# Kernel tuning notes

Measured on AMD Instinct MI355X. Metric: run time of the kernel, lower is better.

The kernel has to match this reference:

```python
import math
import jax, jax.numpy as jnp
import numpy as np

HEAD_DIM = 64
CAUSAL = True


def setup_inputs() -> dict:
    key = jax.random.key(0)
    kq, kk, kv = jax.random.split(key, 3)
    q = jax.random.normal(kq, (2, 16, 1024, HEAD_DIM), dtype=jnp.float32)
    k = jax.random.normal(kk, (2, 16, 8192, HEAD_DIM), dtype=jnp.float32)
    v = jax.random.normal(kv, (2, 16, 8192, HEAD_DIM), dtype=jnp.float32)
    return {"q": q, "k": k, "v": v, "q_chunk_start": 7168}


def reference(q, k, v, q_chunk_start):
    # q: (B, nh, Tq, dh); k, v: (B, nh, Tk, dh)
    Tq = q.shape[2]
    Tk = k.shape[2]
    scale = math.sqrt(HEAD_DIM)
    # scores: (B, nh, Tq, Tk)
    scores = jnp.einsum("bhqd,bhkd->bhqk", q, k) / scale
    if CAUSAL:
        q_pos = jnp.arange(Tq) + q_chunk_start          # (Tq,)
        k_pos = jnp.arange(Tk)                          # (Tk,)
        mask = k_pos[None, :] > q_pos[:, None]          # (Tq, Tk) True = masked
        scores = jnp.where(mask, -jnp.inf, scores)
    attn = jax.nn.softmax(scores, axis=-1)
    attn = jnp.nan_to_num(attn, nan=0.0)                # fully-masked rows -> 0
    return jnp.einsum("bhqk,bhkd->bhqd", attn, v)
```

## Files before the change

kernel.cpp:

```cpp
#include <hip/hip_runtime.h>
#include <hip/hip_bf16.h>

#define TQ 1024
#define TK 8192
#define DH 64
#define NBH 32
#define QT 64
#define KT 64
#define NW 4

typedef __attribute__((ext_vector_type(8))) short short8;
typedef __attribute__((ext_vector_type(4))) short short4v;
typedef __attribute__((ext_vector_type(4))) float f32x4;

static __device__ __forceinline__ short f2bf(float f) {
  __hip_bfloat16 h = __float2bfloat16(f);
  return __builtin_bit_cast(short, h);
}

__global__ __launch_bounds__(256, 2)
void attn_fwd(const float* __restrict__ qg,
              const float* __restrict__ kg,
              const float* __restrict__ vg,
              const int* __restrict__ qcs_p,
              float* __restrict__ outg)
{
  __shared__ __align__(16) short Klds[KT * DH];
  __shared__ __align__(16) short Vt[DH * KT];
  __shared__ __align__(16) short Plds[NW][16 * KT];

  const int tid  = threadIdx.x;
  const int wave = tid >> 6;
  const int lane = tid & 63;
  const int lg   = lane >> 4;
  const int li   = lane & 15;

  const int bid = blockIdx.x;
  const int bh  = bid & (NBH - 1);
  const int qt  = bid >> 5;
  const int qcs = *qcs_p;

  const int q_base = qt * QT;
  const int wrow   = wave * 16;

  const float* qp = qg + ((size_t)bh * TQ + q_base + wrow) * DH;
  const float* kp = kg + (size_t)bh * TK * DH;
  const float* vp = vg + (size_t)bh * TK * DH;

  const float qscale = 0.125f * 1.44269504088896f;
  short8 qf[2];
  #pragma unroll
  for (int h = 0; h < 2; ++h) {
    const float* src = qp + li * DH + h * 32 + lg * 8;
    float4 a = *(const float4*)(src);
    float4 b = *(const float4*)(src + 4);
    short8 f;
    f[0] = f2bf(a.x * qscale); f[1] = f2bf(a.y * qscale);
    f[2] = f2bf(a.z * qscale); f[3] = f2bf(a.w * qscale);
    f[4] = f2bf(b.x * qscale); f[5] = f2bf(b.y * qscale);
    f[6] = f2bf(b.z * qscale); f[7] = f2bf(b.w * qscale);
    qf[h] = f;
  }

  f32x4 o[4];
  #pragma unroll
  for (int ct = 0; ct < 4; ++ct) o[ct] = (f32x4){0.f, 0.f, 0.f, 0.f};
  float rm[4], rl[4];
  #pragma unroll
  for (int r = 0; r < 4; ++r) { rm[r] = -1e30f; rl[r] = 0.f; }

  const int lim    = qcs + q_base + QT;
  const int n_keys = lim < TK ? lim : TK;
  const int n_tiles = (n_keys + KT - 1) / KT;

  const int t_key = tid >> 4;
  const int t_d   = (tid & 15) * 4;

  for (int tile = 0; tile < n_tiles; ++tile) {
    const int kt0 = tile * KT;

    #pragma unroll
    for (int it = 0; it < 4; ++it) {
      const int key = t_key + it * 16;
      const size_t goff = (size_t)(kt0 + key) * DH + t_d;
      float4 kv = *(const float4*)(kp + goff);
      short4v ks;
      ks[0] = f2bf(kv.x); ks[1] = f2bf(kv.y);
      ks[2] = f2bf(kv.z); ks[3] = f2bf(kv.w);
      int e = (key * DH + t_d) ^ ((key & 7) << 3);
      *(short4v*)(&Klds[e]) = ks;

      float4 vv = *(const float4*)(vp + goff);
      short vs0 = f2bf(vv.x), vs1 = f2bf(vv.y), vs2 = f2bf(vv.z), vs3 = f2bf(vv.w);
      int d0 = t_d;
      Vt[((d0 + 0) * KT + key) ^ (((d0 + 0) & 7) << 3)] = vs0;
      Vt[((d0 + 1) * KT + key) ^ (((d0 + 1) & 7) << 3)] = vs1;
      Vt[((d0 + 2) * KT + key) ^ (((d0 + 2) & 7) << 3)] = vs2;
      Vt[((d0 + 3) * KT + key) ^ (((d0 + 3) & 7) << 3)] = vs3;
    }
    __syncthreads();

    f32x4 s[4];
    #pragma unroll
    for (int t = 0; t < 4; ++t) {
      f32x4 acc = (f32x4){0.f, 0.f, 0.f, 0.f};
      #pragma unroll
      for (int h = 0; h < 2; ++h) {
        int e = ((t * 16 + li) * DH + h * 32 + lg * 8) ^ ((li & 7) << 3);
        short8 kf = *(const short8*)(&Klds[e]);
        acc = __builtin_amdgcn_mfma_f32_16x16x32_bf16(qf[h], kf, acc, 0, 0, 0);
      }
      s[t] = acc;
    }

    if (kt0 + KT - 1 > qcs + q_base + wrow) {
      #pragma unroll
      for (int t = 0; t < 4; ++t) {
        const int keyg = kt0 + t * 16 + li;
        #pragma unroll
        for (int r = 0; r < 4; ++r) {
          const int qpos = qcs + q_base + wrow + lg * 4 + r;
          if (keyg > qpos) s[t][r] = -INFINITY;
        }
      }
    }

    float al[4], mn[4];
    #pragma unroll
    for (int r = 0; r < 4; ++r) {
      float tm = fmaxf(fmaxf(s[0][r], s[1][r]), fmaxf(s[2][r], s[3][r]));
      #pragma unroll
      for (int off = 1; off < 16; off <<= 1)
        tm = fmaxf(tm, __shfl_xor(tm, off, 64));
      float m2 = fmaxf(rm[r], tm);
      al[r] = __builtin_amdgcn_exp2f(rm[r] - m2);
      mn[r] = m2;
      rm[r] = m2;
    }

    float ps[4] = {0.f, 0.f, 0.f, 0.f};
    #pragma unroll
    for (int t = 0; t < 4; ++t) {
      #pragma unroll
      for (int r = 0; r < 4; ++r) {
        float p = __builtin_amdgcn_exp2f(s[t][r] - mn[r]);
        ps[r] += p;
        const int row = lg * 4 + r;
        Plds[wave][(row * KT + t * 16 + li) ^ ((row & 7) << 3)] = f2bf(p);
      }
    }

    #pragma unroll
    for (int r = 0; r < 4; ++r) {
      float sum = ps[r];
      #pragma unroll
      for (int off = 1; off < 16; off <<= 1)
        sum += __shfl_xor(sum, off, 64);
      rl[r] = rl[r] * al[r] + sum;
      #pragma unroll
      for (int ct = 0; ct < 4; ++ct) o[ct][r] *= al[r];
    }

    #pragma unroll
    for (int sk = 0; sk < 2; ++sk) {
      int ep = (li * KT + sk * 32 + lg * 8) ^ ((li & 7) << 3);
      short8 pf = *(const short8*)(&Plds[wave][ep]);
      #pragma unroll
      for (int ct = 0; ct < 4; ++ct) {
        int ev = ((ct * 16 + li) * KT + sk * 32 + lg * 8) ^ ((li & 7) << 3);
        short8 vf = *(const short8*)(&Vt[ev]);
        o[ct] = __builtin_amdgcn_mfma_f32_16x16x32_bf16(pf, vf, o[ct], 0, 0, 0);
      }
    }
    __syncthreads();
  }

  float* op = outg + ((size_t)bh * TQ + q_base + wrow) * DH;
  #pragma unroll
  for (int r = 0; r < 4; ++r) {
    const float inv = rl[r] > 0.f ? 1.0f / rl[r] : 0.f;
    #pragma unroll
    for (int ct = 0; ct < 4; ++ct) {
      op[(lg * 4 + r) * DH + ct * 16 + li] = o[ct][r] * inv;
    }
  }
}

extern "C" void kernel_launch(void* const* d_in, const int* in_sizes, int n_in,
                              void* d_out, int out_size, void* d_ws, size_t ws_size,
                              hipStream_t stream) {
  const float* q   = (const float*)d_in[0];
  const float* k   = (const float*)d_in[1];
  const float* v   = (const float*)d_in[2];
  const int*   qcs = (const int*)d_in[3];
  float* out = (float*)d_out;

  dim3 grid(NBH * (TQ / QT));
  dim3 block(256);
  attn_fwd<<<grid, block, 0, stream>>>(q, k, v, qcs, out);
}
```

Before: 438.4 us.

## Split key dimension into four chunks with a separate combine kernel

Turns the attention into a split-K (flash-decoding style) scheme. Each block handles one quarter of the key range and writes unnormalized partial outputs plus row max and sum to workspace, and a second kernel merges them with log-sum-exp weights. The aim is to raise the grid from 512 to 2048 blocks so the GPU stays busy, since each block otherwise walks up to 8192 keys serially. It also raises the occupancy hint in launch bounds and changes the V-transpose LDS swizzle to cut bank conflicts. The cost is extra workspace traffic and a second launch, with a fallback to the old single-kernel path when the workspace is too small.

Measured after the change: 945.7 us. 2.16x slower.

```diff
diff --git a/kernel.cpp b/kernel.cpp
--- a/kernel.cpp
+++ b/kernel.cpp
@@ -8,6 +8,7 @@
 #define QT 64
 #define KT 64
 #define NW 4
+#define ROWS (NBH * TQ)
 
 typedef __attribute__((ext_vector_type(8))) short short8;
 typedef __attribute__((ext_vector_type(4))) short short4v;
@@ -18,12 +19,15 @@
   return __builtin_bit_cast(short, h);
 }
 
-__global__ __launch_bounds__(256, 2)
+template<int NS, bool PART>
+__global__ __launch_bounds__(256, 6)
 void attn_fwd(const float* __restrict__ qg,
               const float* __restrict__ kg,
               const float* __restrict__ vg,
               const int* __restrict__ qcs_p,
-              float* __restrict__ outg)
+              float* __restrict__ outg,
+              float* __restrict__ mpart,
+              float* __restrict__ lpart)
 {
   __shared__ __align__(16) short Klds[KT * DH];
   __shared__ __align__(16) short Vt[DH * KT];
@@ -37,11 +41,14 @@
 
   const int bid = blockIdx.x;
   const int bh  = bid & (NBH - 1);
-  const int qt  = bid >> 5;
+  const int s   = (bid >> 5) & (NS - 1);
+  const int qt  = bid >> (5 + (NS == 4 ? 2 : 0));
   const int qcs = *qcs_p;
 
   const int q_base = qt * QT;
   const int wrow   = wave * 16;
+  const int chunk_start = s * (TK / NS);
+  const int chunk_end   = chunk_start + (TK / NS);
 
   const float* qp = qg + ((size_t)bh * TQ + q_base + wrow) * DH;
   const float* kp = kg + (size_t)bh * TK * DH;
@@ -69,15 +76,15 @@
   #pragma unroll
   for (int r = 0; r < 4; ++r) { rm[r] = -1e30f; rl[r] = 0.f; }
 
-  const int lim    = qcs + q_base + QT;
-  const int n_keys = lim < TK ? lim : TK;
-  const int n_tiles = (n_keys + KT - 1) / KT;
+  int lim = qcs + q_base + QT;
+  if (lim > chunk_end) lim = chunk_end;
+  const int n_tiles = (lim - chunk_start + KT - 1) / KT;
 
   const int t_key = tid >> 4;
   const int t_d   = (tid & 15) * 4;
 
   for (int tile = 0; tile < n_tiles; ++tile) {
-    const int kt0 = tile * KT;
+    const int kt0 = chunk_start + tile * KT;
 
     #pragma unroll
     for (int it = 0; it < 4; ++it) {
@@ -93,14 +100,14 @@
       float4 vv = *(const float4*)(vp + goff);
       short vs0 = f2bf(vv.x), vs1 = f2bf(vv.y), vs2 = f2bf(vv.z), vs3 = f2bf(vv.w);
       int d0 = t_d;
-      Vt[((d0 + 0) * KT + key) ^ (((d0 + 0) & 7) << 3)] = vs0;
-      Vt[((d0 + 1) * KT + key) ^ (((d0 + 1) & 7) << 3)] = vs1;
-      Vt[((d0 + 2) * KT + key) ^ (((d0 + 2) & 7) << 3)] = vs2;
-      Vt[((d0 + 3) * KT + key) ^ (((d0 + 3) & 7) << 3)] = vs3;
+      Vt[((d0 + 0) * KT + key) ^ ((((d0 + 0) >> 1) & 7) << 3)] = vs0;
+      Vt[((d0 + 1) * KT + key) ^ ((((d0 + 1) >> 1) & 7) << 3)] = vs1;
+      Vt[((d0 + 2) * KT + key) ^ ((((d0 + 2) >> 1) & 7) << 3)] = vs2;
+      Vt[((d0 + 3) * KT + key) ^ ((((d0 + 3) >> 1) & 7) << 3)] = vs3;
     }
     __syncthreads();
 
-    f32x4 s[4];
+    f32x4 sv[4];
     #pragma unroll
     for (int t = 0; t < 4; ++t) {
       f32x4 acc = (f32x4){0.f, 0.f, 0.f, 0.f};
@@ -110,7 +117,7 @@
         short8 kf = *(const short8*)(&Klds[e]);
         acc = __builtin_amdgcn_mfma_f32_16x16x32_bf16(qf[h], kf, acc, 0, 0, 0);
       }
-      s[t] = acc;
+      sv[t] = acc;
     }
 
     if (kt0 + KT - 1 > qcs + q_base + wrow) {
@@ -120,7 +127,7 @@
         #pragma unroll
         for (int r = 0; r < 4; ++r) {
           const int qpos = qcs + q_base + wrow + lg * 4 + r;
-          if (keyg > qpos) s[t][r] = -INFINITY;
+          if (keyg > qpos) sv[t][r] = -INFINITY;
         }
       }
     }
@@ -128,7 +135,7 @@
     float al[4], mn[4];
     #pragma unroll
     for (int r = 0; r < 4; ++r) {
-      float tm = fmaxf(fmaxf(s[0][r], s[1][r]), fmaxf(s[2][r], s[3][r]));
+      float tm = fmaxf(fmaxf(sv[0][r], sv[1][r]), fmaxf(sv[2][r], sv[3][r]));
       #pragma unroll
       for (int off = 1; off < 16; off <<= 1)
         tm = fmaxf(tm, __shfl_xor(tm, off, 64));
@@ -143,7 +150,7 @@
     for (int t = 0; t < 4; ++t) {
       #pragma unroll
       for (int r = 0; r < 4; ++r) {
-        float p = __builtin_amdgcn_exp2f(s[t][r] - mn[r]);
+        float p = __builtin_amdgcn_exp2f(sv[t][r] - mn[r]);
         ps[r] += p;
         const int row = lg * 4 + r;
         Plds[wave][(row * KT + t * 16 + li) ^ ((row & 7) << 3)] = f2bf(p);
@@ -167,7 +174,8 @@
       short8 pf = *(const short8*)(&Plds[wave][ep]);
       #pragma unroll
       for (int ct = 0; ct < 4; ++ct) {
-        int ev = ((ct * 16 + li) * KT + sk * 32 + lg * 8) ^ ((li & 7) << 3);
+        int d = ct * 16 + li;
+        int ev = (d * KT + sk * 32 + lg * 8) ^ (((d >> 1) & 7) << 3);
         short8 vf = *(const short8*)(&Vt[ev]);
         o[ct] = __builtin_amdgcn_mfma_f32_16x16x32_bf16(pf, vf, o[ct], 0, 0, 0);
       }
@@ -175,15 +183,58 @@
     __syncthreads();
   }
 
-  float* op = outg + ((size_t)bh * TQ + q_base + wrow) * DH;
-  #pragma unroll
-  for (int r = 0; r < 4; ++r) {
-    const float inv = rl[r] > 0.f ? 1.0f / rl[r] : 0.f;
-    #pragma unroll
-    for (int ct = 0; ct < 4; ++ct) {
-      op[(lg * 4 + r) * DH + ct * 16 + li] = o[ct][r] * inv;
-    }
-  }
+  if constexpr (PART) {
+    float* opr = outg + (((size_t)s * NBH + bh) * TQ + q_base + wrow) * DH;
+    const size_t rbase = ((size_t)s * NBH + bh) * TQ + q_base + wrow;
+    #pragma unroll
+    for (int r = 0; r < 4; ++r) {
+      #pragma unroll
+      for (int ct = 0; ct < 4; ++ct)
+        opr[(lg * 4 + r) * DH + ct * 16 + li] = o[ct][r];
+      if (li == 0) {
+        mpart[rbase + lg * 4 + r] = rm[r];
+        lpart[rbase + lg * 4 + r] = rl[r];
+      }
+    }
+  } else {
+    float* op = outg + ((size_t)bh * TQ + q_base + wrow) * DH;
+    #pragma unroll
+    for (int r = 0; r < 4; ++r) {
+      const float inv = rl[r] > 0.f ? 1.0f / rl[r] : 0.f;
+      #pragma unroll
+      for (int ct = 0; ct < 4; ++ct)
+        op[(lg * 4 + r) * DH + ct * 16 + li] = o[ct][r] * inv;
+    }
+  }
+}
+
+template<int NS>
+__global__ __launch_bounds__(256)
+void combine(const float* __restrict__ opart,
+             const float* __restrict__ mp,
+             const float* __restrict__ lp,
+             float* __restrict__ outg)
+{
+  const int gid = blockIdx.x * 256 + threadIdx.x;
+  const int rg = gid >> 6;
+  const int d  = gid & 63;
+
+  float m[NS], l[NS];
+  float M = -1e30f;
+  #pragma unroll
+  for (int s = 0; s < NS; ++s) {
+    m[s] = mp[(size_t)s * ROWS + rg];
+    l[s] = lp[(size_t)s * ROWS + rg];
+    M = fmaxf(M, m[s]);
+  }
+  float L = 0.f, acc = 0.f;
+  #pragma unroll
+  for (int s = 0; s < NS; ++s) {
+    float w = __builtin_amdgcn_exp2f(m[s] - M);
+    L += w * l[s];
+    acc += w * opart[((size_t)s * ROWS + rg) * DH + d];
+  }
+  outg[(size_t)rg * DH + d] = L > 0.f ? acc / L : 0.f;
 }
 
 extern "C" void kernel_launch(void* const* d_in, const int* in_sizes, int n_in,
@@ -195,7 +246,20 @@
   const int*   qcs = (const int*)d_in[3];
   float* out = (float*)d_out;
 
-  dim3 grid(NBH * (TQ / QT));
-  dim3 block(256);
-  attn_fwd<<<grid, block, 0, stream>>>(q, k, v, qcs, out);
-}
+  constexpr int    NS = 4;
+  constexpr size_t O_ELEMS  = (size_t)NS * ROWS * DH;
+  constexpr size_t ML_ELEMS = (size_t)NS * ROWS;
+  constexpr size_t WS_NEED  = (O_ELEMS + 2 * ML_ELEMS) * sizeof(float);
+
+  if (ws_size >= WS_NEED) {
+    float* opart = (float*)d_ws;
+    float* mpart = opart + O_ELEMS;
+    float* lpart = mpart + ML_ELEMS;
+    dim3 grid(NBH * NS * (TQ / QT));
+    attn_fwd<NS, true><<<grid, dim3(256), 0, stream>>>(q, k, v, qcs, opart, mpart, lpart);
+    combine<NS><<<dim3(ROWS * DH / 256), dim3(256), 0, stream>>>(opart, mpart, lpart, out);
+  } else {
+    dim3 grid(NBH * (TQ / QT));
+    attn_fwd<1, false><<<grid, dim3(256), 0, stream>>>(q, k, v, qcs, out, nullptr, nullptr);
+  }
+}
```

## Pre-convert K/V to swizzled bf16 tiles and double-buffer via global_load_lds

Applied to the files above, without the earlier changes.

Adds a prep kernel that converts K and V from fp32 to bf16 once, writing each 64x64 tile in the final swizzled LDS layout (V transposed) into workspace. The main kernel then streams the tiles straight into double-buffered LDS with global_load_lds, prefetching the next tile during compute, and raises wave priority around the MFMA sections. This removes the repeated per-block fp32 loads and conversions (each K/V tile is reread by 16 query-tile blocks) and overlaps memory with compute. The cost is an extra kernel launch plus writing and rereading a bf16 copy, and doubled K/V LDS use. A fallback path with a different V swizzle is kept for when workspace is too small.

New measurement: 383.0 us. 1.14x faster.

```diff
diff --git a/kernel.cpp b/kernel.cpp
--- a/kernel.cpp
+++ b/kernel.cpp
@@ -8,6 +8,8 @@
 #define QT 64
 #define KT 64
 #define NW 4
+#define NTILE (TK / KT)
+#define TILE_E (KT * DH)
 
 typedef __attribute__((ext_vector_type(8))) short short8;
 typedef __attribute__((ext_vector_type(4))) short short4v;
@@ -18,15 +20,58 @@
   return __builtin_bit_cast(short, h);
 }
 
+#define GLD16(gsrc, ldst)                                                     \
+  __builtin_amdgcn_global_load_lds(                                           \
+      (const __attribute__((address_space(1))) unsigned int*)(gsrc),          \
+      (__attribute__((address_space(3))) unsigned int*)(ldst), 16, 0, 0)
+
+__global__ __launch_bounds__(256)
+void prep(const float* __restrict__ kg, const float* __restrict__ vg,
+          short* __restrict__ Kg2, short* __restrict__ Vg2)
+{
+  __shared__ __align__(16) short Ki[TILE_E];
+  __shared__ __align__(16) short Vi[TILE_E];
+  const int bid = blockIdx.x;
+  const int h = bid >> 7, t = bid & (NTILE - 1);
+  const int tid = threadIdx.x;
+  const int t_key = tid >> 4;
+  const int t_d   = (tid & 15) * 4;
+
+  const float* kp = kg + ((size_t)h * TK + (size_t)t * KT) * DH;
+  const float* vp = vg + ((size_t)h * TK + (size_t)t * KT) * DH;
+
+  #pragma unroll
+  for (int it = 0; it < 4; ++it) {
+    const int key = t_key + it * 16;
+    float4 kv = *(const float4*)(kp + key * DH + t_d);
+    short4v ks;
+    ks[0] = f2bf(kv.x); ks[1] = f2bf(kv.y); ks[2] = f2bf(kv.z); ks[3] = f2bf(kv.w);
+    *(short4v*)(&Ki[(key * 64 + t_d) ^ ((key & 7) << 3)]) = ks;
+
+    float4 vv = *(const float4*)(vp + key * DH + t_d);
+    Vi[((t_d + 0) * 64 + key) ^ (((t_d + 0) & 7) << 3)] = f2bf(vv.x);
+    Vi[((t_d + 1) * 64 + key) ^ (((t_d + 1) & 7) << 3)] = f2bf(vv.y);
+    Vi[((t_d + 2) * 64 + key) ^ (((t_d + 2) & 7) << 3)] = f2bf(vv.z);
+    Vi[((t_d + 3) * 64 + key) ^ (((t_d + 3) & 7) << 3)] = f2bf(vv.w);
+  }
+  __syncthreads();
+
+  const size_t base = (size_t)bid * TILE_E;
+  *(short8*)(&Kg2[base + tid * 16])     = *(short8*)(&Ki[tid * 16]);
+  *(short8*)(&Kg2[base + tid * 16 + 8]) = *(short8*)(&Ki[tid * 16 + 8]);
+  *(short8*)(&Vg2[base + tid * 16])     = *(short8*)(&Vi[tid * 16]);
+  *(short8*)(&Vg2[base + tid * 16 + 8]) = *(short8*)(&Vi[tid * 16 + 8]);
+}
+
 __global__ __launch_bounds__(256, 2)
-void attn_fwd(const float* __restrict__ qg,
-              const float* __restrict__ kg,
-              const float* __restrict__ vg,
-              const int* __restrict__ qcs_p,
-              float* __restrict__ outg)
+void attn_main(const float* __restrict__ qg,
+               const short* __restrict__ Kg2,
+               const short* __restrict__ Vg2,
+               const int* __restrict__ qcs_p,
+               float* __restrict__ outg)
 {
-  __shared__ __align__(16) short Klds[KT * DH];
-  __shared__ __align__(16) short Vt[DH * KT];
+  __shared__ __align__(16) short Kb[2][TILE_E];
+  __shared__ __align__(16) short Vb[2][TILE_E];
   __shared__ __align__(16) short Plds[NW][16 * KT];
 
   const int tid  = threadIdx.x;
@@ -44,8 +89,7 @@
   const int wrow   = wave * 16;
 
   const float* qp = qg + ((size_t)bh * TQ + q_base + wrow) * DH;
-  const float* kp = kg + (size_t)bh * TK * DH;
-  const float* vp = vg + (size_t)bh * TK * DH;
+  const size_t tile_base0 = (size_t)bh * NTILE * TILE_E;
 
   const float qscale = 0.125f * 1.44269504088896f;
   short8 qf[2];
@@ -73,45 +117,38 @@
   const int n_keys = lim < TK ? lim : TK;
   const int n_tiles = (n_keys + KT - 1) / KT;
 
-  const int t_key = tid >> 4;
-  const int t_d   = (tid & 15) * 4;
+  const int chunk = wave * 2;
+
+  auto stage = [&](int b, int tile) {
+    const size_t tb = tile_base0 + (size_t)tile * TILE_E;
+    GLD16(Kg2 + tb + (chunk + 0) * 512 + lane * 8, &Kb[b][(chunk + 0) * 512]);
+    GLD16(Kg2 + tb + (chunk + 1) * 512 + lane * 8, &Kb[b][(chunk + 1) * 512]);
+    GLD16(Vg2 + tb + (chunk + 0) * 512 + lane * 8, &Vb[b][(chunk + 0) * 512]);
+    GLD16(Vg2 + tb + (chunk + 1) * 512 + lane * 8, &Vb[b][(chunk + 1) * 512]);
+  };
+
+  stage(0, 0);
+  __syncthreads();
+  int buf = 0;
 
   for (int tile = 0; tile < n_tiles; ++tile) {
     const int kt0 = tile * KT;
-
-    #pragma unroll
-    for (int it = 0; it < 4; ++it) {
-      const int key = t_key + it * 16;
-      const size_t goff = (size_t)(kt0 + key) * DH + t_d;
-      float4 kv = *(const float4*)(kp + goff);
-      short4v ks;
-      ks[0] = f2bf(kv.x); ks[1] = f2bf(kv.y);
-      ks[2] = f2bf(kv.z); ks[3] = f2bf(kv.w);
-      int e = (key * DH + t_d) ^ ((key & 7) << 3);
-      *(short4v*)(&Klds[e]) = ks;
-
-      float4 vv = *(const float4*)(vp + goff);
-      short vs0 = f2bf(vv.x), vs1 = f2bf(vv.y), vs2 = f2bf(vv.z), vs3 = f2bf(vv.w);
-      int d0 = t_d;
-      Vt[((d0 + 0) * KT + key) ^ (((d0 + 0) & 7) << 3)] = vs0;
-      Vt[((d0 + 1) * KT + key) ^ (((d0 + 1) & 7) << 3)] = vs1;
-      Vt[((d0 + 2) * KT + key) ^ (((d0 + 2) & 7) << 3)] = vs2;
-      Vt[((d0 + 3) * KT + key) ^ (((d0 + 3) & 7) << 3)] = vs3;
-    }
-    __syncthreads();
-
-    f32x4 s[4];
+    if (tile + 1 < n_tiles) stage(buf ^ 1, tile + 1);
+
+    f32x4 sv[4];
+    __builtin_amdgcn_s_setprio(1);
     #pragma unroll
     for (int t = 0; t < 4; ++t) {
       f32x4 acc = (f32x4){0.f, 0.f, 0.f, 0.f};
       #pragma unroll
       for (int h = 0; h < 2; ++h) {
-        int e = ((t * 16 + li) * DH + h * 32 + lg * 8) ^ ((li & 7) << 3);
-        short8 kf = *(const short8*)(&Klds[e]);
+        int e = ((t * 16 + li) * 64 + h * 32 + lg * 8) ^ ((li & 7) << 3);
+        short8 kf = *(const short8*)(&Kb[buf][e]);
         acc = __builtin_amdgcn_mfma_f32_16x16x32_bf16(qf[h], kf, acc, 0, 0, 0);
       }
-      s[t] = acc;
-    }
+      sv[t] = acc;
+    }
+    __builtin_amdgcn_s_setprio(0);
 
     if (kt0 + KT - 1 > qcs + q_base + wrow) {
       #pragma unroll
@@ -120,7 +157,7 @@
         #pragma unroll
         for (int r = 0; r < 4; ++r) {
           const int qpos = qcs + q_base + wrow + lg * 4 + r;
-          if (keyg > qpos) s[t][r] = -INFINITY;
+          if (keyg > qpos) sv[t][r] = -INFINITY;
         }
       }
     }
@@ -128,7 +165,7 @@
     float al[4], mn[4];
     #pragma unroll
     for (int r = 0; r < 4; ++r) {
-      float tm = fmaxf(fmaxf(s[0][r], s[1][r]), fmaxf(s[2][r], s[3][r]));
+      float tm = fmaxf(fmaxf(sv[0][r], sv[1][r]), fmaxf(sv[2][r], sv[3][r]));
       #pragma unroll
       for (int off = 1; off < 16; off <<= 1)
         tm = fmaxf(tm, __shfl_xor(tm, off, 64));
@@ -143,7 +180,7 @@
     for (int t = 0; t < 4; ++t) {
       #pragma unroll
       for (int r = 0; r < 4; ++r) {
-        float p = __builtin_amdgcn_exp2f(s[t][r] - mn[r]);
+        float p = __builtin_amdgcn_exp2f(sv[t][r] - mn[r]);
         ps[r] += p;
         const int row = lg * 4 + r;
         Plds[wave][(row * KT + t * 16 + li) ^ ((row & 7) << 3)] = f2bf(p);
@@ -165,9 +202,176 @@
     for (int sk = 0; sk < 2; ++sk) {
       int ep = (li * KT + sk * 32 + lg * 8) ^ ((li & 7) << 3);
       short8 pf = *(const short8*)(&Plds[wave][ep]);
+      __builtin_amdgcn_s_setprio(1);
       #pragma unroll
       for (int ct = 0; ct < 4; ++ct) {
-        int ev = ((ct * 16 + li) * KT + sk * 32 + lg * 8) ^ ((li & 7) << 3);
+        int e = ((ct * 16 + li) * 64 + sk * 32 + lg * 8) ^ ((li & 7) << 3);
+        short8 vf = *(const short8*)(&Vb[buf][e]);
+        o[ct] = __builtin_amdgcn_mfma_f32_16x16x32_bf16(pf, vf, o[ct], 0, 0, 0);
+      }
+      __builtin_amdgcn_s_setprio(0);
+    }
+
+    __syncthreads();
+    buf ^= 1;
+  }
+
+  float* op = outg + ((size_t)bh * TQ + q_base + wrow) * DH;
+  #pragma unroll
+  for (int r = 0; r < 4; ++r) {
+    const float inv = rl[r] > 0.f ? 1.0f / rl[r] : 0.f;
+    #pragma unroll
+    for (int ct = 0; ct < 4; ++ct)
+      op[(lg * 4 + r) * DH + ct * 16 + li] = o[ct][r] * inv;
+  }
+}
+
+__global__ __launch_bounds__(256, 2)
+void attn_fallback(const float* __restrict__ qg,
+                   const float* __restrict__ kg,
+                   const float* __restrict__ vg,
+                   const int* __restrict__ qcs_p,
+                   float* __restrict__ outg)
+{
+  __shared__ __align__(16) short Klds[KT * DH];
+  __shared__ __align__(16) short Vt[DH * KT];
+  __shared__ __align__(16) short Plds[NW][16 * KT];
+
+  const int tid  = threadIdx.x;
+  const int wave = tid >> 6;
+  const int lane = tid & 63;
+  const int lg   = lane >> 4;
+  const int li   = lane & 15;
+
+  const int bid = blockIdx.x;
+  const int bh  = bid & (NBH - 1);
+  const int qt  = bid >> 5;
+  const int qcs = *qcs_p;
+
+  const int q_base = qt * QT;
+  const int wrow   = wave * 16;
+
+  const float* qp = qg + ((size_t)bh * TQ + q_base + wrow) * DH;
+  const float* kp = kg + (size_t)bh * TK * DH;
+  const float* vp = vg + (size_t)bh * TK * DH;
+
+  const float qscale = 0.125f * 1.44269504088896f;
+  short8 qf[2];
+  #pragma unroll
+  for (int h = 0; h < 2; ++h) {
+    const float* src = qp + li * DH + h * 32 + lg * 8;
+    float4 a = *(const float4*)(src);
+    float4 b = *(const float4*)(src + 4);
+    short8 f;
+    f[0] = f2bf(a.x * qscale); f[1] = f2bf(a.y * qscale);
+    f[2] = f2bf(a.z * qscale); f[3] = f2bf(a.w * qscale);
+    f[4] = f2bf(b.x * qscale); f[5] = f2bf(b.y * qscale);
+    f[6] = f2bf(b.z * qscale); f[7] = f2bf(b.w * qscale);
+    qf[h] = f;
+  }
+
+  f32x4 o[4];
+  #pragma unroll
+  for (int ct = 0; ct < 4; ++ct) o[ct] = (f32x4){0.f, 0.f, 0.f, 0.f};
+  float rm[4], rl[4];
+  #pragma unroll
+  for (int r = 0; r < 4; ++r) { rm[r] = -1e30f; rl[r] = 0.f; }
+
+  const int lim    = qcs + q_base + QT;
+  const int n_keys = lim < TK ? lim : TK;
+  const int n_tiles = (n_keys + KT - 1) / KT;
+
+  const int t_key = tid >> 4;
+  const int t_d   = (tid & 15) * 4;
+
+  for (int tile = 0; tile < n_tiles; ++tile) {
+    const int kt0 = tile * KT;
+    #pragma unroll
+    for (int it = 0; it < 4; ++it) {
+      const int key = t_key + it * 16;
+      const size_t goff = (size_t)(kt0 + key) * DH + t_d;
+      float4 kv = *(const float4*)(kp + goff);
+      short4v ks;
+      ks[0] = f2bf(kv.x); ks[1] = f2bf(kv.y); ks[2] = f2bf(kv.z); ks[3] = f2bf(kv.w);
+      *(short4v*)(&Klds[(key * DH + t_d) ^ ((key & 7) << 3)]) = ks;
+
+      float4 vv = *(const float4*)(vp + goff);
+      Vt[((t_d + 0) * KT + key) ^ ((((t_d + 0) >> 1) & 7) << 3)] = f2bf(vv.x);
+      Vt[((t_d + 1) * KT + key) ^ ((((t_d + 1) >> 1) & 7) << 3)] = f2bf(vv.y);
+      Vt[((t_d + 2) * KT + key) ^ ((((t_d + 2) >> 1) & 7) << 3)] = f2bf(vv.z);
+      Vt[((t_d + 3) * KT + key) ^ ((((t_d + 3) >> 1) & 7) << 3)] = f2bf(vv.w);
+    }
+    __syncthreads();
+
+    f32x4 sv[4];
+    #pragma unroll
+    for (int t = 0; t < 4; ++t) {
+      f32x4 acc = (f32x4){0.f, 0.f, 0.f, 0.f};
+      #pragma unroll
+      for (int h = 0; h < 2; ++h) {
+        int e = ((t * 16 + li) * DH + h * 32 + lg * 8) ^ ((li & 7) << 3);
+        short8 kf = *(const short8*)(&Klds[e]);
+        acc = __builtin_amdgcn_mfma_f32_16x16x32_bf16(qf[h], kf, acc, 0, 0, 0);
+      }
+      sv[t] = acc;
+    }
+
+    if (kt0 + KT - 1 > qcs + q_base + wrow) {
+      #pragma unroll
+      for (int t = 0; t < 4; ++t) {
+        const int keyg = kt0 + t * 16 + li;
+        #pragma unroll
+        for (int r = 0; r < 4; ++r) {
+          const int qpos = qcs + q_base + wrow + lg * 4 + r;
+          if (keyg > qpos) sv[t][r] = -INFINITY;
+        }
+      }
+    }
+
+    float al[4], mn[4];
+    #pragma unroll
+    for (int r = 0; r < 4; ++r) {
+      float tm = fmaxf(fmaxf(sv[0][r], sv[1][r]), fmaxf(sv[2][r], sv[3][r]));
+      #pragma unroll
+      for (int off = 1; off < 16; off <<= 1)
+        tm = fmaxf(tm, __shfl_xor(tm, off, 64));
+      float m2 = fmaxf(rm[r], tm);
+      al[r] = __builtin_amdgcn_exp2f(rm[r] - m2);
+      mn[r] = m2;
+      rm[r] = m2;
+    }
+
+    float ps[4] = {0.f, 0.f, 0.f, 0.f};
+    #pragma unroll
+    for (int t = 0; t < 4; ++t) {
+      #pragma unroll
+      for (int r = 0; r < 4; ++r) {
+        float p = __builtin_amdgcn_exp2f(sv[t][r] - mn[r]);
+        ps[r] += p;
+        const int row = lg * 4 + r;
+        Plds[wave][(row * KT + t * 16 + li) ^ ((row & 7) << 3)] = f2bf(p);
+      }
+    }
+
+    #pragma unroll
+    for (int r = 0; r < 4; ++r) {
+      float sum = ps[r];
+      #pragma unroll
+      for (int off = 1; off < 16; off <<= 1)
+        sum += __shfl_xor(sum, off, 64);
+      rl[r] = rl[r] * al[r] + sum;
+      #pragma unroll
+      for (int ct = 0; ct < 4; ++ct) o[ct][r] *= al[r];
+    }
+
+    #pragma unroll
+    for (int sk = 0; sk < 2; ++sk) {
+      int ep = (li * KT + sk * 32 + lg * 8) ^ ((li & 7) << 3);
+      short8 pf = *(const short8*)(&Plds[wave][ep]);
+      #pragma unroll
+      for (int ct = 0; ct < 4; ++ct) {
+        int d = ct * 16 + li;
+        int ev = (d * KT + sk * 32 + lg * 8) ^ (((d >> 1) & 7) << 3);
         short8 vf = *(const short8*)(&Vt[ev]);
         o[ct] = __builtin_amdgcn_mfma_f32_16x16x32_bf16(pf, vf, o[ct], 0, 0, 0);
       }
@@ -180,9 +384,8 @@
   for (int r = 0; r < 4; ++r) {
     const float inv = rl[r] > 0.f ? 1.0f / rl[r] : 0.f;
     #pragma unroll
-    for (int ct = 0; ct < 4; ++ct) {
+    for (int ct = 0; ct < 4; ++ct)
       op[(lg * 4 + r) * DH + ct * 16 + li] = o[ct][r] * inv;
-    }
   }
 }
 
@@ -195,7 +398,15 @@
   const int*   qcs = (const int*)d_in[3];
   float* out = (float*)d_out;
 
-  dim3 grid(NBH * (TQ / QT));
-  dim3 block(256);
-  attn_fwd<<<grid, block, 0, stream>>>(q, k, v, qcs, out);
+  constexpr size_t IMG_ELEMS = (size_t)NBH * NTILE * TILE_E;
+  constexpr size_t WS_NEED   = 2 * IMG_ELEMS * sizeof(short);
+
+  if (ws_size >= WS_NEED) {
+    short* Kg2 = (short*)d_ws;
+    short* Vg2 = Kg2 + IMG_ELEMS;
+    prep<<<dim3(NBH * NTILE), dim3(256), 0, stream>>>(k, v, Kg2, Vg2);
+    attn_main<<<dim3(NBH * (TQ / QT)), dim3(256), 0, stream>>>(q, Kg2, Vg2, qcs, out);
+  } else {
+    attn_fallback<<<dim3(NBH * (TQ / QT)), dim3(256), 0, stream>>>(q, k, v, qcs, out);
+  }
 }
```
